# Kernel optimization log

Measured on AMD Instinct MI355X. Metric: run time of the kernel, lower is better.

The kernel has to match this reference:

```python
import jax, jax.numpy as jnp
import numpy as np

B, C, H, W = 4, 64, 128, 128
G, K, PAD, DIL = 4, 3, 2, 2  # deformable conv config
OFF_CH = 2 * K * K * G  # 72


def conv2d(x, w, b, pad):
    out = jax.lax.conv_general_dilated(
        x, w, window_strides=(1, 1), padding=[(pad, pad), (pad, pad)],
        dimension_numbers=('NCHW', 'OIHW', 'NCHW'))
    return out + b[None, :, None, None]


def deform_conv(x, offset, w, b):
    # DCNv1 (no modulation mask), groups=G, offset_groups=G, torchvision semantics.
    Bn, Cn, Hn, Wn = x.shape
    Cg = Cn // G
    Cout = w.shape[0]
    Coutg = Cout // G
    # offset channels laid out as [G, K*K, (dy,dx)]
    off = offset.reshape(Bn, G, K * K, 2, Hn, Wn)
    dy, dx = off[:, :, :, 0], off[:, :, :, 1]  # [B,G,9,H,W]
    kk = jnp.arange(K * K)
    gy = (jnp.arange(Hn)[None, :] - PAD + DIL * (kk // K)[:, None]).astype(x.dtype)[:, :, None]  # [9,H,1]
    gx = (jnp.arange(Wn)[None, :] - PAD + DIL * (kk % K)[:, None]).astype(x.dtype)[:, None, :]   # [9,1,W]
    py = dy + gy[None, None]  # [B,G,9,H,W]
    px = dx + gx[None, None]
    xg = x.reshape(Bn, G, Cg, Hn, Wn)

    def gather(img, py_, px_):  # img [Cg,H,W]; py_,px_ [9,H,W]
        y0 = jnp.floor(py_)
        x0 = jnp.floor(px_)
        ly = py_ - y0
        lx = px_ - x0

        def corner(iy, ix, wgt):
            valid = (iy >= 0) & (iy <= Hn - 1) & (ix >= 0) & (ix <= Wn - 1)
            iyc = jnp.clip(iy, 0, Hn - 1).astype(jnp.int32)
            ixc = jnp.clip(ix, 0, Wn - 1).astype(jnp.int32)
            return img[:, iyc, ixc] * (wgt * valid)[None]

        return (corner(y0, x0, (1 - ly) * (1 - lx))
                + corner(y0, x0 + 1, (1 - ly) * lx)
                + corner(y0 + 1, x0, ly * (1 - lx))
                + corner(y0 + 1, x0 + 1, ly * lx))

    sampled = jax.vmap(jax.vmap(gather))(xg, py, px)  # [B,G,Cg,9,H,W]
    wr = w.reshape(G, Coutg, Cg, K * K)
    out = jnp.einsum('bgckhw,gock->bgohw', sampled, wr).reshape(Bn, Cout, Hn, Wn)
    return out + b[None, :, None, None]


def setup_inputs() -> dict:
    key = jax.random.key(0)
    ks = jax.random.split(key, 32)
    f32 = jnp.float32
    d = {
        'Fref': jax.random.normal(ks[0], (B, C, H, W), f32),
        'Fmov1': jax.random.normal(ks[1], (B, C, H, W), f32),
        'Fmov2': jax.random.normal(ks[2], (B, C, H, W), f32),
        'cr_w': jax.random.normal(ks[3], (64, 128, 3, 3), f32) * 0.05,
        'cr_b': jax.random.normal(ks[4], (64,), f32) * 0.05,
    }
    i = 5
    for name in ('off1', 'off2', 'off3', 'off4'):
        d[name + '_w'] = jax.random.normal(ks[i], (OFF_CH, 64, 3, 3), f32) * 0.01
        d[name + '_b'] = jax.random.normal(ks[i + 1], (OFF_CH,), f32) * 0.01
        i += 2
    for name in ('d1', 'd2', 'd3', 'd4'):
        d[name + '_w'] = jax.random.normal(ks[i], (64, 64 // G, 3, 3), f32) * 0.05
        d[name + '_b'] = jax.random.normal(ks[i + 1], (64,), f32) * 0.05
        i += 2
    return d


def reference(Fref, Fmov1, Fmov2, cr_w, cr_b,
              off1_w, off1_b, off2_w, off2_b, off3_w, off3_b, off4_w, off4_b,
              d1_w, d1_b, d2_w, d2_b, d3_w, d3_b, d4_w, d4_b):
    def align(fr, fm):
        fea = conv2d(jnp.concatenate([fr, fm], axis=1), cr_w, cr_b, 1)
        fea = deform_conv(fea, conv2d(fea, off1_w, off1_b, 1), d1_w, d1_b)
        fea = deform_conv(fea, conv2d(fea, off2_w, off2_b, 1), d2_w, d2_b)
        off3 = conv2d(fea, off3_w, off3_b, 1)
        fea = deform_conv(fm, off3, d3_w, d3_b)  # note: deform3 applied to Fmov, per source
        out = deform_conv(fea, conv2d(fea, off4_w, off4_b, 1), d4_w, d4_b)
        return out

    return (align(Fref, Fmov1), align(Fref, Fmov2))
```

## Files before the change

### kernel.cpp

```cpp
#include <hip/hip_runtime.h>


using f16   = _Float16;
using f16x8 = __attribute__((ext_vector_type(8))) f16;
using h2    = __attribute__((ext_vector_type(2))) f16;
using u16x8 = __attribute__((ext_vector_type(8))) unsigned short;
using f32x4 = __attribute__((ext_vector_type(4))) float;

static constexpr int Hh = 128, Ww = 128, NB = 4, NPIX = Hh * Ww;
static constexpr int BB = 8;

__device__ __forceinline__ unsigned short f2h(float f) {
  f16 h = (f16)f;
  return *(unsigned short*)&h;
}

struct PrepPtrs {
  const float* cw[5];
  unsigned short* cd[5];
  const float* dw[4];
  unsigned short* dd[4];
  const float* ob[4];
  float* obd[4];
};

__global__ __launch_bounds__(256) void prep_all_kernel(PrepPtrs pp) {
  const int which = blockIdx.y;
  const int i = blockIdx.x * 256 + threadIdx.x;
  if (which == 0) {
    if (i >= 9 * 64 * 128) return;
    const int cin = 128, cop = 64;
    const int ci = i % cin, co = (i / cin) % cop, t = i / (cin * cop);
    pp.cd[0][i] = f2h(pp.cw[0][((size_t)co * cin + ci) * 9 + t]);
  } else if (which <= 4) {
    if (i >= 9 * 80 * 64) return;
    const int cin = 64, cop = 80;
    const int ci = i % cin, co = (i / cin) % cop, t = i / (cin * cop);
    const int g = co / 20, c = co % 20;
    float v = (c < 18) ? pp.cw[which][((size_t)(g * 18 + c) * cin + ci) * 9 + t]
                       : 0.f;
    pp.cd[which][i] = f2h(v);
  } else if (which <= 8) {
    if (i >= 4 * 5 * 16 * 32) return;
    const int kk = i & 31, o = (i >> 5) & 15, pair = (i >> 9) % 5;
    const int g = i / 2560;
    const int t = pair * 2 + (kk >> 4), c = kk & 15;
    float v = (t < 9) ? pp.dw[which - 5][(size_t)((g * 16 + o) * 16 + c) * 9 + t]
                      : 0.f;
    pp.dd[which - 5][i] = f2h(v);
  } else {
    if (i >= 4 * 80) return;
    const int ten = i / 80, co = i % 80;
    const int g = co / 20, c = co % 20;
    pp.obd[ten][co] = (c < 18) ? pp.ob[ten][g * 18 + c] : 0.f;
  }
}

__global__ __launch_bounds__(256) void to_gs_kernel(
    const float* __restrict__ Fref, const float* __restrict__ Fm1,
    const float* __restrict__ Fm2, unsigned short* __restrict__ frefG,
    unsigned short* __restrict__ fmovG) {
  const int t = blockIdx.x * 256 + threadIdx.x;
  const int b2 = t >> 14, pix = t & (NPIX - 1);
  const float* fm = (b2 < 4 ? Fm1 : Fm2) + (size_t)(b2 & 3) * 64 * NPIX + pix;
  for (int c8 = 0; c8 < 8; ++c8) {
    u16x8 v;
#pragma unroll
    for (int j = 0; j < 8; ++j) v[j] = f2h(fm[(size_t)(c8 * 8 + j) * NPIX]);
    *(u16x8*)(fmovG + ((size_t)(b2 * 4 + (c8 >> 1)) * NPIX + pix) * 16 +
              (c8 & 1) * 8) = v;
  }
  if (b2 < 4) {
    const float* fr = Fref + (size_t)b2 * 64 * NPIX + pix;
    for (int c8 = 0; c8 < 8; ++c8) {
      u16x8 v;
#pragma unroll
      for (int j = 0; j < 8; ++j) v[j] = f2h(fr[(size_t)(c8 * 8 + j) * NPIX]);
      *(u16x8*)(frefG + ((size_t)(b2 * 4 + (c8 >> 1)) * NPIX + pix) * 16 +
                (c8 & 1) * 8) = v;
    }
  }
}

template <int CIN, int COP, int CO_REAL, int OST, bool OUT_GS, bool OFF_GS>
__global__ __launch_bounds__(512) void convmfma_kernel(
    const unsigned short* __restrict__ in0, int bmask0,
    const unsigned short* __restrict__ in1, int bmask1,
    const unsigned short* __restrict__ wT,
    const float* __restrict__ biasP,
    unsigned short* __restrict__ out) {
  constexpr int COF = COP / 16;
  constexpr int NCH = CIN / 64;
  __shared__ unsigned short sA[9 * COP * 64];
  __shared__ unsigned short sB[324 * 64];

  const int tile = blockIdx.x, b = blockIdx.y;
  const int ty0 = (tile >> 3) << 4, tx0 = (tile & 7) << 4;
  const int tid = threadIdx.x;
  const int wv = tid >> 6, l = tid & 63;
  const int lm = l & 15, lq = l >> 4;

  f32x4 acc[COF][2];
#pragma unroll
  for (int cf = 0; cf < COF; ++cf)
#pragma unroll
    for (int pf = 0; pf < 2; ++pf) acc[cf][pf] = (f32x4){0.f, 0.f, 0.f, 0.f};

  const unsigned short* base0 = in0 + (size_t)(b & bmask0) * 4 * NPIX * 16;
  const unsigned short* base1 =
      (NCH > 1) ? in1 + (size_t)(b & bmask1) * 4 * NPIX * 16 : nullptr;

  for (int ch = 0; ch < NCH; ++ch) {
    const unsigned short* inB = (ch == 0) ? base0 : base1;
    for (int q = tid; q < 324 * 8; q += 512) {
      const int pix = q >> 3, ci8 = q & 7;
      const int r = pix / 18, c = pix - r * 18;
      const int gy = ty0 - 1 + r, gx = tx0 - 1 + c;
      u16x8 v;
      if (gy >= 0 && gy < Hh && gx >= 0 && gx < Ww) {
        v = *(const u16x8*)(inB + ((size_t)(ci8 >> 1) * NPIX + gy * Ww + gx) *
                                      16 + (ci8 & 1) * 8);
      } else {
#pragma unroll
        for (int j = 0; j < 8; ++j) v[j] = 0;
      }
      const int boff = pix * 128 + ((ci8 * 16) ^ ((pix & 7) << 4));
      *(u16x8*)((char*)sB + boff) = v;
    }
    for (int q = tid; q < 9 * COP * 8; q += 512) {
      const int ci8 = q & 7;
      const int co = (q >> 3) % COP;
      const int t = q / (8 * COP);
      u16x8 v = *(const u16x8*)(wT + (size_t)(t * COP + co) * CIN + ch * 64 +
                                ci8 * 8);
      const int aoff = (t * COP + co) * 128 + ((ci8 * 16) ^ ((co & 7) << 4));
      *(u16x8*)((char*)sA + aoff) = v;
    }
    __syncthreads();
    for (int t = 0; t < 9; ++t) {
      const int dy = t / 3, dx = t - dy * 3;
#pragma unroll
      for (int kc = 0; kc < 2; ++kc) {
        f16x8 afr[COF];
#pragma unroll
        for (int cf = 0; cf < COF; ++cf) {
          const int co = cf * 16 + lm;
          const int aoff =
              (t * COP + co) * 128 + ((kc * 64 + lq * 16) ^ ((co & 7) << 4));
          afr[cf] = *(const f16x8*)((const char*)sA + aoff);
        }
#pragma unroll
        for (int pf = 0; pf < 2; ++pf) {
          const int pix = wv * 32 + pf * 16 + lm;
          const int spix = ((pix >> 4) + dy) * 18 + (pix & 15) + dx;
          const int boff =
              spix * 128 + ((kc * 64 + lq * 16) ^ ((spix & 7) << 4));
          const f16x8 bfr = *(const f16x8*)((const char*)sB + boff);
#pragma unroll
          for (int cf = 0; cf < COF; ++cf)
            acc[cf][pf] = __builtin_amdgcn_mfma_f32_16x16x32_f16(
                afr[cf], bfr, acc[cf][pf], 0, 0, 0);
        }
      }
    }
    __syncthreads();
  }
  unsigned short* outB = out + (size_t)b * NPIX * OST;
#pragma unroll
  for (int cf = 0; cf < COF; ++cf) {
    const int co0 = cf * 16 + lq * 4;
    if (co0 >= CO_REAL) continue;
    const float4 bv = *(const float4*)(biasP + co0);
#pragma unroll
    for (int pf = 0; pf < 2; ++pf) {
      const int pix = wv * 32 + pf * 16 + lm;
      const int gpix = (ty0 + (pix >> 4)) * Ww + tx0 + (pix & 15);
      const f32x4 v = acc[cf][pf];
      ushort4 pk;
      pk.x = f2h(v[0] + bv.x);
      pk.y = f2h(v[1] + bv.y);
      pk.z = f2h(v[2] + bv.z);
      pk.w = f2h(v[3] + bv.w);
      if (OUT_GS) {
        *(ushort4*)(out + ((size_t)(b * 4 + cf) * NPIX + gpix) * 16 + lq * 4) =
            pk;
      } else if (OFF_GS) {
        const int gg = co0 / 20, cc = co0 % 20;
        *(ushort4*)(out + ((size_t)(b * 4 + gg) * NPIX + gpix) * 20 + cc) = pk;
      } else {
        *(ushort4*)(outB + (size_t)gpix * OST + co0) = pk;
      }
    }
  }
}

template <bool NCHW_OUT>
__global__ __launch_bounds__(256, 4) void deform13_kernel(
    const unsigned short* __restrict__ x,
    const unsigned short* __restrict__ off,
    const unsigned short* __restrict__ dwP,
    const float* __restrict__ bias,
    float* __restrict__ outF, unsigned short* __restrict__ outH) {
  __shared__ char sB[128 * 80];
  const int tile = blockIdx.x, g = blockIdx.y, b = blockIdx.z;
  const int ty0 = (tile >> 2) << 2;
  const int tx0 = (tile & 3) << 5;
  const int tid = threadIdx.x;
  const int p = tid >> 1, h = tid & 1;
  const int l = tid & 63, wv = tid >> 6;
  const int lm = l & 15, lq = l >> 4;
  const int y = ty0 + (p >> 5), xx = tx0 + (p & 31);

  const unsigned short* xP = x + (size_t)(b * 4 + g) * NPIX * 16 + h * 8;
  const unsigned short* offP =
      off + ((size_t)(b * 4 + g) * NPIX + y * Ww + xx) * 20;

  unsigned od[9];
#pragma unroll
  for (int t = 0; t < 9; ++t) od[t] = *(const unsigned*)(offP + 2 * t);

  f16x8 afr[5];
#pragma unroll
  for (int pr = 0; pr < 5; ++pr)
    afr[pr] = *(const f16x8*)(dwP + ((size_t)(g * 5 + pr) * 16 + lm) * 32 +
                              lq * 8);

  f32x4 acc[2];
  acc[0] = (f32x4){0.f, 0.f, 0.f, 0.f};
  acc[1] = (f32x4){0.f, 0.f, 0.f, 0.f};

  char* myB = sB + p * 80 + h * 16;

#pragma unroll
  for (int pair = 0; pair < 5; ++pair) {
#pragma unroll
    for (int ti = 0; ti < 2; ++ti) {
      const int t = pair * 2 + ti;
      uint4 sv = (uint4){0u, 0u, 0u, 0u};
      if (t < 9) {
        const unsigned odw = od[t];
        const f16* op = (const f16*)&odw;
        const float dy = (float)op[0];
        const float dx = (float)op[1];
        const float py = dy + (float)(y - 2 + 2 * (t / 3));
        const float px = dx + (float)(xx - 2 + 2 * (t % 3));
        const float fy = floorf(py), fx = floorf(px);
        const int y0 = (int)fy, x0 = (int)fx;
        const int y1 = y0 + 1, x1 = x0 + 1;
        const float ly = py - fy, lx = px - fx;
        float w00 = (1.f - ly) * (1.f - lx), w01 = (1.f - ly) * lx;
        float w10 = ly * (1.f - lx), w11 = ly * lx;
        const bool vy0 = (y0 >= 0) && (y0 < Hh), vy1 = (y1 >= 0) && (y1 < Hh);
        const bool vx0 = (x0 >= 0) && (x0 < Ww), vx1 = (x1 >= 0) && (x1 < Ww);
        w00 = (vy0 && vx0) ? w00 : 0.f;
        w01 = (vy0 && vx1) ? w01 : 0.f;
        w10 = (vy1 && vx0) ? w10 : 0.f;
        w11 = (vy1 && vx1) ? w11 : 0.f;
        const int y0c = min(max(y0, 0), Hh - 1), y1c = min(max(y1, 0), Hh - 1);
        const int x0c = min(max(x0, 0), Ww - 1), x1c = min(max(x1, 0), Ww - 1);
        const u16x8 a00 = *(const u16x8*)(xP + (size_t)(y0c * Ww + x0c) * 16);
        const u16x8 a01 = *(const u16x8*)(xP + (size_t)(y0c * Ww + x1c) * 16);
        const u16x8 a10 = *(const u16x8*)(xP + (size_t)(y1c * Ww + x0c) * 16);
        const u16x8 a11 = *(const u16x8*)(xP + (size_t)(y1c * Ww + x1c) * 16);
        const h2* c00 = (const h2*)&a00;
        const h2* c01 = (const h2*)&a01;
        const h2* c10 = (const h2*)&a10;
        const h2* c11 = (const h2*)&a11;
        const f16 h00 = (f16)w00, h01 = (f16)w01;
        const f16 h10 = (f16)w10, h11 = (f16)w11;
        const h2 p00 = (h2){h00, h00}, p01 = (h2){h01, h01};
        const h2 p10 = (h2){h10, h10}, p11 = (h2){h11, h11};
        unsigned fw[4];
#pragma unroll
        for (int j = 0; j < 4; ++j) {
          h2 r = c00[j] * p00;
          r += c01[j] * p01;
          r += c10[j] * p10;
          r += c11[j] * p11;
          fw[j] = *(const unsigned*)&r;
        }
        sv = (uint4){fw[0], fw[1], fw[2], fw[3]};
      }
      *(uint4*)(myB + ti * 32) = sv;
    }
#pragma unroll
    for (int n = 0; n < 2; ++n) {
      const f16x8 bfr =
          *(const f16x8*)(sB + (wv * 32 + n * 16 + lm) * 80 + lq * 16);
      acc[n] = __builtin_amdgcn_mfma_f32_16x16x32_f16(afr[pair], bfr, acc[n],
                                                      0, 0, 0);
    }
  }

  const float4 bv = *(const float4*)(bias + g * 16 + lq * 4);
#pragma unroll
  for (int n = 0; n < 2; ++n) {
    const int pixl = wv * 32 + n * 16 + lm;
    const int gpix = (ty0 + (pixl >> 5)) * Ww + tx0 + (pixl & 31);
    const f32x4 v = acc[n];
    if (NCHW_OUT) {
      float* oB = outF + (size_t)(b * 64 + g * 16 + lq * 4) * NPIX + gpix;
      oB[0] = v[0] + bv.x;
      oB[NPIX] = v[1] + bv.y;
      oB[2 * NPIX] = v[2] + bv.z;
      oB[3 * NPIX] = v[3] + bv.w;
    } else {
      ushort4 pk;
      pk.x = f2h(v[0] + bv.x);
      pk.y = f2h(v[1] + bv.y);
      pk.z = f2h(v[2] + bv.z);
      pk.w = f2h(v[3] + bv.w);
      *(ushort4*)(outH + ((size_t)(b * 4 + g) * NPIX + gpix) * 16 + lq * 4) =
          pk;
    }
  }
}


extern "C" void kernel_launch(void* const* d_in, const int* in_sizes, int n_in,
                              void* d_out, int out_size, void* d_ws,
                              size_t ws_size, hipStream_t stream) {
  const float* Fref = (const float*)d_in[0];
  const float* Fmov1 = (const float*)d_in[1];
  const float* Fmov2 = (const float*)d_in[2];
  const float* cr_w = (const float*)d_in[3];
  const float* cr_b = (const float*)d_in[4];
  const float* offw[4] = {(const float*)d_in[5], (const float*)d_in[7],
                          (const float*)d_in[9], (const float*)d_in[11]};
  const float* offb[4] = {(const float*)d_in[6], (const float*)d_in[8],
                          (const float*)d_in[10], (const float*)d_in[12]};
  const float* dw[4] = {(const float*)d_in[13], (const float*)d_in[15],
                        (const float*)d_in[17], (const float*)d_in[19]};
  const float* db[4] = {(const float*)d_in[14], (const float*)d_in[16],
                        (const float*)d_in[18], (const float*)d_in[20]};

  char* p = (char*)d_ws;
  auto carve = [&](size_t bytes) {
    void* r = p;
    p += (bytes + 255) & ~(size_t)255;
    return r;
  };
  unsigned short* frefG = (unsigned short*)carve((size_t)4 * 4 * NPIX * 16 * 2);
  unsigned short* fmovG = (unsigned short*)carve((size_t)BB * 4 * NPIX * 16 * 2);
  unsigned short* feaA = (unsigned short*)carve((size_t)BB * 4 * NPIX * 16 * 2);
  unsigned short* feaB = (unsigned short*)carve((size_t)BB * 4 * NPIX * 16 * 2);
  unsigned short* offB = (unsigned short*)carve((size_t)BB * 4 * NPIX * 20 * 2);
  unsigned short* wcrT = (unsigned short*)carve((size_t)9 * 64 * 128 * 2);
  unsigned short* woffT[4];
  for (int i = 0; i < 4; ++i)
    woffT[i] = (unsigned short*)carve((size_t)9 * 80 * 64 * 2);
  unsigned short* dwP[4];
  for (int i = 0; i < 4; ++i)
    dwP[i] = (unsigned short*)carve((size_t)4 * 5 * 16 * 32 * 2);
  float* obP[4];
  for (int i = 0; i < 4; ++i) obP[i] = (float*)carve((size_t)80 * 4);

  PrepPtrs pp;
  pp.cw[0] = cr_w;
  pp.cd[0] = wcrT;
  for (int i = 0; i < 4; ++i) {
    pp.cw[i + 1] = offw[i];
    pp.cd[i + 1] = woffT[i];
    pp.dw[i] = dw[i];
    pp.dd[i] = dwP[i];
    pp.ob[i] = offb[i];
    pp.obd[i] = obP[i];
  }
  prep_all_kernel<<<dim3(288, 10), 256, 0, stream>>>(pp);

  to_gs_kernel<<<BB * NPIX / 256, 256, 0, stream>>>(Fref, Fmov1, Fmov2, frefG,
                                                    fmovG);

  const dim3 cgrid(64, BB), cblk(512);
  const dim3 dgrid(128, 4, BB), dblk(256);
  float* outF = (float*)d_out;

  convmfma_kernel<128, 64, 64, 0, true, false><<<cgrid, cblk, 0, stream>>>(
      frefG, 3, fmovG, 7, wcrT, cr_b, feaA);
  convmfma_kernel<64, 80, 80, 20, false, true><<<cgrid, cblk, 0, stream>>>(
      feaA, 7, nullptr, 0, woffT[0], obP[0], offB);
  deform13_kernel<false>
      <<<dgrid, dblk, 0, stream>>>(feaA, offB, dwP[0], db[0], nullptr, feaB);
  convmfma_kernel<64, 80, 80, 20, false, true><<<cgrid, cblk, 0, stream>>>(
      feaB, 7, nullptr, 0, woffT[1], obP[1], offB);
  deform13_kernel<false>
      <<<dgrid, dblk, 0, stream>>>(feaB, offB, dwP[1], db[1], nullptr, feaA);
  convmfma_kernel<64, 80, 80, 20, false, true><<<cgrid, cblk, 0, stream>>>(
      feaA, 7, nullptr, 0, woffT[2], obP[2], offB);
  deform13_kernel<false>
      <<<dgrid, dblk, 0, stream>>>(fmovG, offB, dwP[2], db[2], nullptr, feaB);
  convmfma_kernel<64, 80, 80, 20, false, true><<<cgrid, cblk, 0, stream>>>(
      feaB, 7, nullptr, 0, woffT[3], obP[3], offB);
  deform13_kernel<true>
      <<<dgrid, dblk, 0, stream>>>(feaB, offB, dwP[3], db[3], outF, nullptr);
}
```

Measured before the change: 277.8 us.

## Stream conv weights per tap through double-buffered LDS to raise occupancy

Replaces the full 9-tap weight tile in shared memory with a two-slot per-tap weight buffer that is refilled while the current tap is computed, and adds a min-blocks hint to launch bounds. The aim is to cut LDS use per block so more 512-thread blocks fit per CU and weight-load latency overlaps with MFMA work. In exchange it adds a __syncthreads per tap and small global weight loads inside the main loop, and the occupancy hint may force register spills.

```diff
diff --git a/kernel.cpp b/kernel.cpp
--- a/kernel.cpp
+++ b/kernel.cpp
@@ -83,7 +83,7 @@
 }
 
 template <int CIN, int COP, int CO_REAL, int OST, bool OUT_GS, bool OFF_GS>
-__global__ __launch_bounds__(512) void convmfma_kernel(
+__global__ __launch_bounds__(512, 4) void convmfma_kernel(
     const unsigned short* __restrict__ in0, int bmask0,
     const unsigned short* __restrict__ in1, int bmask1,
     const unsigned short* __restrict__ wT,
@@ -91,7 +91,8 @@
     unsigned short* __restrict__ out) {
   constexpr int COF = COP / 16;
   constexpr int NCH = CIN / 64;
-  __shared__ unsigned short sA[9 * COP * 64];
+  constexpr int NT = NCH * 9;
+  __shared__ unsigned short sW[2][COP * 64];
   __shared__ unsigned short sB[324 * 64];
 
   const int tile = blockIdx.x, b = blockIdx.y;
@@ -110,7 +111,7 @@
   const unsigned short* base1 =
       (NCH > 1) ? in1 + (size_t)(b & bmask1) * 4 * NPIX * 16 : nullptr;
 
-  for (int ch = 0; ch < NCH; ++ch) {
+  auto stage_input = [&](int ch) {
     const unsigned short* inB = (ch == 0) ? base0 : base1;
     for (int q = tid; q < 324 * 8; q += 512) {
       const int pix = q >> 3, ci8 = q & 7;
@@ -127,44 +128,59 @@
       const int boff = pix * 128 + ((ci8 * 16) ^ ((pix & 7) << 4));
       *(u16x8*)((char*)sB + boff) = v;
     }
-    for (int q = tid; q < 9 * COP * 8; q += 512) {
+  };
+  auto stage_w = [&](int tt, int buf) {
+    const int ch = tt / 9, t = tt - ch * 9;
+    for (int q = tid; q < COP * 8; q += 512) {
       const int ci8 = q & 7;
-      const int co = (q >> 3) % COP;
-      const int t = q / (8 * COP);
+      const int co = q >> 3;
       u16x8 v = *(const u16x8*)(wT + (size_t)(t * COP + co) * CIN + ch * 64 +
                                 ci8 * 8);
-      const int aoff = (t * COP + co) * 128 + ((ci8 * 16) ^ ((co & 7) << 4));
-      *(u16x8*)((char*)sA + aoff) = v;
+      const int aoff = co * 128 + ((ci8 * 16) ^ ((co & 7) << 4));
+      *(u16x8*)((char*)sW[buf] + aoff) = v;
+    }
+  };
+
+  stage_input(0);
+  stage_w(0, 0);
+  __syncthreads();
+
+  for (int tt = 0; tt < NT; ++tt) {
+    const int t = tt % 9;
+    const bool nextNewCh = ((tt + 1) % 9 == 0);
+    if (tt + 1 < NT && !nextNewCh) stage_w(tt + 1, (tt + 1) & 1);
+
+    const int dy = t / 3, dx = t - dy * 3;
+    const char* sWc = (const char*)sW[tt & 1];
+#pragma unroll
+    for (int kc = 0; kc < 2; ++kc) {
+      f16x8 afr[COF];
+#pragma unroll
+      for (int cf = 0; cf < COF; ++cf) {
+        const int co = cf * 16 + lm;
+        const int aoff = co * 128 + ((kc * 64 + lq * 16) ^ ((co & 7) << 4));
+        afr[cf] = *(const f16x8*)(sWc + aoff);
+      }
+#pragma unroll
+      for (int pf = 0; pf < 2; ++pf) {
+        const int pix = wv * 32 + pf * 16 + lm;
+        const int spix = ((pix >> 4) + dy) * 18 + (pix & 15) + dx;
+        const int boff = spix * 128 + ((kc * 64 + lq * 16) ^ ((spix & 7) << 4));
+        const f16x8 bfr = *(const f16x8*)((const char*)sB + boff);
+#pragma unroll
+        for (int cf = 0; cf < COF; ++cf)
+          acc[cf][pf] = __builtin_amdgcn_mfma_f32_16x16x32_f16(
+              afr[cf], bfr, acc[cf][pf], 0, 0, 0);
+      }
     }
     __syncthreads();
-    for (int t = 0; t < 9; ++t) {
-      const int dy = t / 3, dx = t - dy * 3;
-#pragma unroll
-      for (int kc = 0; kc < 2; ++kc) {
-        f16x8 afr[COF];
-#pragma unroll
-        for (int cf = 0; cf < COF; ++cf) {
-          const int co = cf * 16 + lm;
-          const int aoff =
-              (t * COP + co) * 128 + ((kc * 64 + lq * 16) ^ ((co & 7) << 4));
-          afr[cf] = *(const f16x8*)((const char*)sA + aoff);
-        }
-#pragma unroll
-        for (int pf = 0; pf < 2; ++pf) {
-          const int pix = wv * 32 + pf * 16 + lm;
-          const int spix = ((pix >> 4) + dy) * 18 + (pix & 15) + dx;
-          const int boff =
-              spix * 128 + ((kc * 64 + lq * 16) ^ ((spix & 7) << 4));
-          const f16x8 bfr = *(const f16x8*)((const char*)sB + boff);
-#pragma unroll
-          for (int cf = 0; cf < COF; ++cf)
-            acc[cf][pf] = __builtin_amdgcn_mfma_f32_16x16x32_f16(
-                afr[cf], bfr, acc[cf][pf], 0, 0, 0);
-        }
-      }
-    }
-    __syncthreads();
-  }
+    if (tt + 1 < NT && nextNewCh) {
+      stage_input((tt + 1) / 9);
+      stage_w(tt + 1, (tt + 1) & 1);
+      __syncthreads();
+    }
+  }
+
   unsigned short* outB = out + (size_t)b * NPIX * OST;
 #pragma unroll
   for (int cf = 0; cf < COF; ++cf) {
```

Result: faster. 257.4 us (-7.3%).
